# Kernel optimization log

Measured on AMD Instinct MI355X. Metric: run time of the kernel, lower is better.

Reference implementation:

```python
import jax, jax.numpy as jnp
import numpy as np

NUM_NODES = 100000
IN_DIM = 64
OUT_DIM = 64
NUM_EDGES = 1250000


def setup_inputs() -> dict:
    key = jax.random.key(0)
    k1, k2, k3, k4, k5 = jax.random.split(key, 5)
    x = jax.random.normal(k1, (NUM_NODES, IN_DIM), dtype=jnp.float32)
    edge_index = jax.random.randint(k2, (2, NUM_EDGES), 0, NUM_NODES, dtype=jnp.int32)
    # Linear params (PyTorch default init: uniform(-1/sqrt(in), 1/sqrt(in)))
    bound = 1.0 / np.sqrt(IN_DIM)
    W_self = jax.random.uniform(k3, (OUT_DIM, IN_DIM), minval=-bound, maxval=bound, dtype=jnp.float32)
    b_self = jax.random.uniform(k4, (OUT_DIM,), minval=-bound, maxval=bound, dtype=jnp.float32)
    W_neigh = jax.random.uniform(k5, (OUT_DIM, IN_DIM), minval=-bound, maxval=bound, dtype=jnp.float32)
    return {"x": x, "edge_index": edge_index, "W_self": W_self, "b_self": b_self, "W_neigh": W_neigh}


def reference(x, edge_index, W_self, b_self, W_neigh):
    # x: [N, D_in], edge_index: [2, E]
    src, dst = edge_index[0], edge_index[1]
    num_nodes = x.shape[0]
    x_src = x[src]  # [E, D_in] gather
    neigh_agg = jax.ops.segment_sum(x_src, dst, num_segments=num_nodes)  # [N, D_in]
    deg = jax.ops.segment_sum(jnp.ones_like(dst, dtype=x.dtype), dst, num_segments=num_nodes)
    deg = jnp.clip(deg, 1.0, None)[:, None]
    neigh_mean = neigh_agg / deg
    out = x @ W_self.T + b_self + neigh_mean @ W_neigh.T
    return jax.nn.relu(out)
```

## Files before the change

kernel.cpp:

```cpp
#include <hip/hip_runtime.h>


#define BKSH 9
#define BKN 512
#define NBMAX 256
#define CAPE 7168
#define WPT (CAPE / BKN)
#define CHUNK 4096
#define EPT (CHUNK / 256)

typedef __attribute__((ext_vector_type(8))) short short8;
typedef __attribute__((ext_vector_type(4))) float floatx4;

static __device__ inline unsigned short f2bf(float f) {
  union { float f; unsigned int u; } v;
  v.f = f;
  unsigned int r = v.u + 0x7FFFu + ((v.u >> 16) & 1u);
  return (unsigned short)(r >> 16);
}

static __device__ inline short8 pack8(float4 a, float4 b) {
  short8 s;
  s[0] = (short)f2bf(a.x); s[1] = (short)f2bf(a.y);
  s[2] = (short)f2bf(a.z); s[3] = (short)f2bf(a.w);
  s[4] = (short)f2bf(b.x); s[5] = (short)f2bf(b.y);
  s[6] = (short)f2bf(b.z); s[7] = (short)f2bf(b.w);
  return s;
}

static __device__ inline void add8(float* a, short8 sv) {
  union { short8 s; unsigned int u[4]; } c; c.s = sv;
#pragma unroll
  for (int i = 0; i < 4; ++i) {
    a[2 * i]     += __uint_as_float(c.u[i] << 16);
    a[2 * i + 1] += __uint_as_float(c.u[i] & 0xFFFF0000u);
  }
}

__global__ __launch_bounds__(256) void k1_main(
    const float* __restrict__ x,
    const float* __restrict__ Wself, const float* __restrict__ bself,
    const float* __restrict__ Wneigh,
    float* __restrict__ yb, unsigned short* __restrict__ zb,
    const int* __restrict__ src, const int* __restrict__ dst,
    int* __restrict__ cursor, int* __restrict__ ebuf,
    int E, int N, int NB, int SCB) {
  __shared__ int h[NBMAX], loff[NBMAX], gbase[NBMAX];
  __shared__ int sbuf[CHUNK];
  int t = threadIdx.x;
  int bid = blockIdx.x;

  if (bid >= SCB) {
    int lane = t & 63;
    int w = t >> 6;
    int tb = (bid - SCB) * 64 + w * 16;
    int m = lane & 15, q = lane >> 4;

    long long rowA = (long long)min(tb + m, N - 1) * 64;
    short8 ax[2];
#pragma unroll
    for (int ks = 0; ks < 2; ++ks) {
      const float* xr = &x[rowA + ks * 32 + q * 8];
      ax[ks] = pack8(*(const float4*)xr, *(const float4*)(xr + 4));
    }

#pragma unroll
    for (int nt = 0; nt < 4; ++nt) {
      int ob = nt * 16;
      long long rowB = (long long)(ob + m) * 64;
      floatx4 accs = {0.f, 0.f, 0.f, 0.f};
      floatx4 accn = {0.f, 0.f, 0.f, 0.f};
#pragma unroll
      for (int ks = 0; ks < 2; ++ks) {
        const float* pw = &Wself[rowB + ks * 32 + q * 8];
        short8 bs = pack8(*(const float4*)pw, *(const float4*)(pw + 4));
        accs = __builtin_amdgcn_mfma_f32_16x16x32_bf16(ax[ks], bs, accs, 0, 0, 0);
        const float* pn = &Wneigh[rowB + ks * 32 + q * 8];
        short8 bn = pack8(*(const float4*)pn, *(const float4*)(pn + 4));
        accn = __builtin_amdgcn_mfma_f32_16x16x32_bf16(ax[ks], bn, accn, 0, 0, 0);
      }
      float bias = bself[ob + m];
#pragma unroll
      for (int r = 0; r < 4; ++r) {
        int node = tb + q * 4 + r;
        if (node < N) {
          yb[(long long)node * 64 + ob + m] = accs[r] + bias;
          zb[(long long)node * 64 + ob + m] = f2bf(accn[r]);
        }
      }
    }
    return;
  }

  if (t < NBMAX) h[t] = 0;
  __syncthreads();

  int base = bid * CHUNK;
  int myd[EPT], mys[EPT];
#pragma unroll
  for (int i = 0; i < EPT; ++i) {
    int e = base + t + 256 * i;
    if (e < E) {
      myd[i] = dst[e];
      mys[i] = src[e];
      atomicAdd(&h[myd[i] >> BKSH], 1);
    } else myd[i] = -1;
  }
  __syncthreads();

  if (t < 64) {
    int i0 = 4 * t;
    int v0 = h[i0], v1 = h[i0 + 1], v2 = h[i0 + 2], v3 = h[i0 + 3];
    int s4 = v0 + v1 + v2 + v3, inc = s4;
#pragma unroll
    for (int off = 1; off < 64; off <<= 1) {
      int u = __shfl_up(inc, off, 64);
      if (t >= off) inc += u;
    }
    int ex = inc - s4;
    loff[i0] = ex; loff[i0 + 1] = ex + v0;
    loff[i0 + 2] = ex + v0 + v1; loff[i0 + 3] = ex + v0 + v1 + v2;
  }
  __syncthreads();

  if (t < NB) {
    if (h[t] > 0) gbase[t] = t * CAPE + atomicAdd(&cursor[t], h[t]);
  }
  if (t < NBMAX) h[t] = 0;
  __syncthreads();

#pragma unroll
  for (int i = 0; i < EPT; ++i) {
    if (myd[i] >= 0) {
      int b = myd[i] >> BKSH;
      int p = atomicAdd(&h[b], 1);
      sbuf[loff[b] + p] = mys[i] | ((myd[i] & (BKN - 1)) << 17);
    }
  }
  __syncthreads();

  int w = t >> 6, lane = t & 63;
  for (int b = w; b < NB; b += 4) {
    int c = h[b], lo = loff[b], go = gbase[b];
    for (int j = lane; j < c; j += 64)
      ebuf[go + j] = sbuf[lo + j];
  }
}

__global__ __launch_bounds__(512) void sb_csr(const int* __restrict__ cursor,
                                              const int* __restrict__ ebuf,
                                              int* __restrict__ col,
                                              int2* __restrict__ rowse, int N) {
  __shared__ int sbuf[CAPE];
  __shared__ int cnt[BKN];
  __shared__ int wsum[8];
  int b = blockIdx.x, t = threadIdx.x;
  int s = b * CAPE;
  int n = cursor[b];
  int e = s + n;

  int my[WPT];
#pragma unroll
  for (int i = 0; i < WPT; ++i) {
    int j = s + t + i * BKN;
    my[i] = (j < e) ? ebuf[j] : -1;
  }

  cnt[t] = 0;
  __syncthreads();
#pragma unroll
  for (int i = 0; i < WPT; ++i)
    if (my[i] >= 0) atomicAdd(&cnt[(my[i] >> 17) & (BKN - 1)], 1);
  __syncthreads();

  int v = cnt[t];
  int lane = t & 63, w = t >> 6;
  int inc = v;
#pragma unroll
  for (int o = 1; o < 64; o <<= 1) {
    int u = __shfl_up(inc, o, 64);
    if (lane >= o) inc += u;
  }
  if (lane == 63) wsum[w] = inc;
  __syncthreads();
  if (t < 8) {
    int s0 = wsum[t], incw = s0;
#pragma unroll
    for (int o = 1; o < 8; o <<= 1) {
      int u = __shfl_up(incw, o, 64);
      if (t >= o) incw += u;
    }
    wsum[t] = incw - s0;
  }
  __syncthreads();
  int ex = wsum[w] + inc - v;
  int node = (b << BKSH) + t;
  if (node < N) rowse[node] = make_int2(s + ex, v);
  __syncthreads();
  cnt[t] = ex;
  __syncthreads();

#pragma unroll
  for (int i = 0; i < WPT; ++i) {
    if (my[i] >= 0) {
      int nl = (my[i] >> 17) & (BKN - 1);
      int p = atomicAdd(&cnt[nl], 1);
      sbuf[p] = my[i] & 0x1FFFF;
    }
  }
  __syncthreads();

  for (int j = t; j < n; j += BKN) col[s + j] = sbuf[j];
}

__global__ __launch_bounds__(256) void gather_final(
    const unsigned short* __restrict__ zb,
    const int2* __restrict__ rowse,
    const int* __restrict__ col,
    const float* __restrict__ yb,
    float* __restrict__ out, int N) {
  int gid = blockIdx.x * 256 + threadIdx.x;
  int node = gid >> 6;
  if (node >= N) return;
  int lane = threadIdx.x & 63;
  int o = lane >> 3, d = lane & 7;
  int2 se = rowse[node];
  int s = se.x, c = se.y, e = s + c;

  float a[8] = {0.f, 0.f, 0.f, 0.f, 0.f, 0.f, 0.f, 0.f};
  float b2[8] = {0.f, 0.f, 0.f, 0.f, 0.f, 0.f, 0.f, 0.f};
  for (int j = s + o; j < e; j += 16) {
    int c0 = col[j];
    bool h2 = (j + 8) < e;
    int c1 = h2 ? col[j + 8] : c0;
    short8 v0 = *(const short8*)&zb[(long long)c0 * 64 + d * 8];
    short8 v1 = *(const short8*)&zb[(long long)c1 * 64 + d * 8];
    add8(a, v0);
    if (h2) add8(b2, v1);
  }
#pragma unroll
  for (int k = 0; k < 8; ++k) a[k] += b2[k];

#pragma unroll
  for (int m = 8; m <= 32; m <<= 1) {
#pragma unroll
    for (int k = 0; k < 8; ++k) a[k] += __shfl_xor(a[k], m, 64);
  }

  if (o == 0) {
    float inv = 1.0f / fmaxf((float)c, 1.0f);
    long long ro = (long long)node * 64 + d * 8;
    float4 y0 = *(const float4*)&yb[ro];
    float4 y1 = *(const float4*)&yb[ro + 4];
    float4 r0, r1;
    r0.x = fmaxf(y0.x + a[0] * inv, 0.f);
    r0.y = fmaxf(y0.y + a[1] * inv, 0.f);
    r0.z = fmaxf(y0.z + a[2] * inv, 0.f);
    r0.w = fmaxf(y0.w + a[3] * inv, 0.f);
    r1.x = fmaxf(y1.x + a[4] * inv, 0.f);
    r1.y = fmaxf(y1.y + a[5] * inv, 0.f);
    r1.z = fmaxf(y1.z + a[6] * inv, 0.f);
    r1.w = fmaxf(y1.w + a[7] * inv, 0.f);
    *(float4*)&out[ro] = r0;
    *(float4*)&out[ro + 4] = r1;
  }
}

extern "C" void kernel_launch(void* const* d_in, const int* in_sizes, int n_in,
                              void* d_out, int out_size, void* d_ws, size_t ws_size,
                              hipStream_t stream) {
  const float* x      = (const float*)d_in[0];
  const int*   eidx   = (const int*)d_in[1];
  const float* Wself  = (const float*)d_in[2];
  const float* bself  = (const float*)d_in[3];
  const float* Wneigh = (const float*)d_in[4];
  float* out = (float*)d_out;

  const int N = in_sizes[0] / 64;
  const int E = in_sizes[1] / 2;
  const int* src = eidx;
  const int* dst = eidx + E;
  const int NB = (N + BKN - 1) / BKN;

  float* yb = (float*)d_ws;
  unsigned short* zb = (unsigned short*)(yb + (size_t)N * 64);
  int* cursor = (int*)(zb + (size_t)N * 64);
  int2* rowse = (int2*)(cursor + NBMAX);
  int* ebuf   = (int*)(rowse + N);
  int* col    = ebuf + (size_t)NB * CAPE;

  hipMemsetAsync(cursor, 0, NBMAX * sizeof(int), stream);

  const int SCB = (E + CHUNK - 1) / CHUNK;
  const int GB = (N + 63) / 64;
  k1_main<<<SCB + GB, 256, 0, stream>>>(x, Wself, bself, Wneigh, yb, zb,
                                        src, dst, cursor, ebuf, E, N, NB, SCB);
  sb_csr<<<NB, BKN, 0, stream>>>(cursor, ebuf, col, rowse, N);
  gather_final<<<(int)(((long long)N * 64 + 255) / 256), 256, 0, stream>>>(
      zb, rowse, col, yb, out, N);
}
```

Before: 163.0 us.

## Replace two-pass bucketed CSR build with degree histogram, scan, and atomic scatter

Replaces the LDS-staged chunk bucketing and per-bucket local sort with a simpler CSR build. Per-node degrees are counted with global atomics, a per-bucket prefix scan produces row starts and cursors, and each edge is placed with a global atomicAdd on its destination cursor. This removes the intermediate ebuf pass and its shared-memory sorting. In exchange it uses 1.25M scattered global atomics, and neighbor order within a row becomes nondeterministic.

```diff
diff --git a/kernel.cpp b/kernel.cpp
--- a/kernel.cpp
+++ b/kernel.cpp
@@ -3,11 +3,8 @@
 
 #define BKSH 9
 #define BKN 512
-#define NBMAX 256
 #define CAPE 7168
-#define WPT (CAPE / BKN)
-#define CHUNK 4096
-#define EPT (CHUNK / 256)
+#define HISTB 512
 
 typedef __attribute__((ext_vector_type(8))) short short8;
 typedef __attribute__((ext_vector_type(4))) float floatx4;
@@ -42,138 +39,66 @@
     const float* __restrict__ Wself, const float* __restrict__ bself,
     const float* __restrict__ Wneigh,
     float* __restrict__ yb, unsigned short* __restrict__ zb,
-    const int* __restrict__ src, const int* __restrict__ dst,
-    int* __restrict__ cursor, int* __restrict__ ebuf,
-    int E, int N, int NB, int SCB) {
-  __shared__ int h[NBMAX], loff[NBMAX], gbase[NBMAX];
-  __shared__ int sbuf[CHUNK];
+    const int* __restrict__ dst, int* __restrict__ deg,
+    int E, int N) {
   int t = threadIdx.x;
   int bid = blockIdx.x;
 
-  if (bid >= SCB) {
-    int lane = t & 63;
-    int w = t >> 6;
-    int tb = (bid - SCB) * 64 + w * 16;
-    int m = lane & 15, q = lane >> 4;
-
-    long long rowA = (long long)min(tb + m, N - 1) * 64;
-    short8 ax[2];
+  if (bid < HISTB) {
+    int stride = HISTB * 256;
+    for (int e = bid * 256 + t; e < E; e += stride)
+      atomicAdd(&deg[dst[e]], 1);
+    return;
+  }
+
+  int lane = t & 63;
+  int w = t >> 6;
+  int tb = (bid - HISTB) * 64 + w * 16;
+  int m = lane & 15, q = lane >> 4;
+
+  long long rowA = (long long)min(tb + m, N - 1) * 64;
+  short8 ax[2];
+#pragma unroll
+  for (int ks = 0; ks < 2; ++ks) {
+    const float* xr = &x[rowA + ks * 32 + q * 8];
+    ax[ks] = pack8(*(const float4*)xr, *(const float4*)(xr + 4));
+  }
+
+#pragma unroll
+  for (int nt = 0; nt < 4; ++nt) {
+    int ob = nt * 16;
+    long long rowB = (long long)(ob + m) * 64;
+    floatx4 accs = {0.f, 0.f, 0.f, 0.f};
+    floatx4 accn = {0.f, 0.f, 0.f, 0.f};
 #pragma unroll
     for (int ks = 0; ks < 2; ++ks) {
-      const float* xr = &x[rowA + ks * 32 + q * 8];
-      ax[ks] = pack8(*(const float4*)xr, *(const float4*)(xr + 4));
+      const float* pw = &Wself[rowB + ks * 32 + q * 8];
+      short8 bs = pack8(*(const float4*)pw, *(const float4*)(pw + 4));
+      accs = __builtin_amdgcn_mfma_f32_16x16x32_bf16(ax[ks], bs, accs, 0, 0, 0);
+      const float* pn = &Wneigh[rowB + ks * 32 + q * 8];
+      short8 bn = pack8(*(const float4*)pn, *(const float4*)(pn + 4));
+      accn = __builtin_amdgcn_mfma_f32_16x16x32_bf16(ax[ks], bn, accn, 0, 0, 0);
     }
-
-#pragma unroll
-    for (int nt = 0; nt < 4; ++nt) {
-      int ob = nt * 16;
-      long long rowB = (long long)(ob + m) * 64;
-      floatx4 accs = {0.f, 0.f, 0.f, 0.f};
-      floatx4 accn = {0.f, 0.f, 0.f, 0.f};
-#pragma unroll
-      for (int ks = 0; ks < 2; ++ks) {
-        const float* pw = &Wself[rowB + ks * 32 + q * 8];
-        short8 bs = pack8(*(const float4*)pw, *(const float4*)(pw + 4));
-        accs = __builtin_amdgcn_mfma_f32_16x16x32_bf16(ax[ks], bs, accs, 0, 0, 0);
-        const float* pn = &Wneigh[rowB + ks * 32 + q * 8];
-        short8 bn = pack8(*(const float4*)pn, *(const float4*)(pn + 4));
-        accn = __builtin_amdgcn_mfma_f32_16x16x32_bf16(ax[ks], bn, accn, 0, 0, 0);
-      }
-      float bias = bself[ob + m];
-#pragma unroll
-      for (int r = 0; r < 4; ++r) {
-        int node = tb + q * 4 + r;
-        if (node < N) {
-          yb[(long long)node * 64 + ob + m] = accs[r] + bias;
-          zb[(long long)node * 64 + ob + m] = f2bf(accn[r]);
-        }
+    float bias = bself[ob + m];
+#pragma unroll
+    for (int r = 0; r < 4; ++r) {
+      int node = tb + q * 4 + r;
+      if (node < N) {
+        yb[(long long)node * 64 + ob + m] = accs[r] + bias;
+        zb[(long long)node * 64 + ob + m] = f2bf(accn[r]);
       }
     }
-    return;
-  }
-
-  if (t < NBMAX) h[t] = 0;
-  __syncthreads();
-
-  int base = bid * CHUNK;
-  int myd[EPT], mys[EPT];
-#pragma unroll
-  for (int i = 0; i < EPT; ++i) {
-    int e = base + t + 256 * i;
-    if (e < E) {
-      myd[i] = dst[e];
-      mys[i] = src[e];
-      atomicAdd(&h[myd[i] >> BKSH], 1);
-    } else myd[i] = -1;
-  }
-  __syncthreads();
-
-  if (t < 64) {
-    int i0 = 4 * t;
-    int v0 = h[i0], v1 = h[i0 + 1], v2 = h[i0 + 2], v3 = h[i0 + 3];
-    int s4 = v0 + v1 + v2 + v3, inc = s4;
-#pragma unroll
-    for (int off = 1; off < 64; off <<= 1) {
-      int u = __shfl_up(inc, off, 64);
-      if (t >= off) inc += u;
-    }
-    int ex = inc - s4;
-    loff[i0] = ex; loff[i0 + 1] = ex + v0;
-    loff[i0 + 2] = ex + v0 + v1; loff[i0 + 3] = ex + v0 + v1 + v2;
-  }
-  __syncthreads();
-
-  if (t < NB) {
-    if (h[t] > 0) gbase[t] = t * CAPE + atomicAdd(&cursor[t], h[t]);
-  }
-  if (t < NBMAX) h[t] = 0;
-  __syncthreads();
-
-#pragma unroll
-  for (int i = 0; i < EPT; ++i) {
-    if (myd[i] >= 0) {
-      int b = myd[i] >> BKSH;
-      int p = atomicAdd(&h[b], 1);
-      sbuf[loff[b] + p] = mys[i] | ((myd[i] & (BKN - 1)) << 17);
-    }
-  }
-  __syncthreads();
-
-  int w = t >> 6, lane = t & 63;
-  for (int b = w; b < NB; b += 4) {
-    int c = h[b], lo = loff[b], go = gbase[b];
-    for (int j = lane; j < c; j += 64)
-      ebuf[go + j] = sbuf[lo + j];
-  }
-}
-
-__global__ __launch_bounds__(512) void sb_csr(const int* __restrict__ cursor,
-                                              const int* __restrict__ ebuf,
-                                              int* __restrict__ col,
-                                              int2* __restrict__ rowse, int N) {
-  __shared__ int sbuf[CAPE];
-  __shared__ int cnt[BKN];
+  }
+}
+
+__global__ __launch_bounds__(512) void bucket_scan(const int* __restrict__ deg,
+                                                   int2* __restrict__ rowse,
+                                                   int* __restrict__ cur, int N) {
   __shared__ int wsum[8];
   int b = blockIdx.x, t = threadIdx.x;
-  int s = b * CAPE;
-  int n = cursor[b];
-  int e = s + n;
-
-  int my[WPT];
-#pragma unroll
-  for (int i = 0; i < WPT; ++i) {
-    int j = s + t + i * BKN;
-    my[i] = (j < e) ? ebuf[j] : -1;
-  }
-
-  cnt[t] = 0;
-  __syncthreads();
-#pragma unroll
-  for (int i = 0; i < WPT; ++i)
-    if (my[i] >= 0) atomicAdd(&cnt[(my[i] >> 17) & (BKN - 1)], 1);
-  __syncthreads();
-
-  int v = cnt[t];
+  int node = (b << BKSH) + t;
+  int v = (node < N) ? deg[node] : 0;
+
   int lane = t & 63, w = t >> 6;
   int inc = v;
 #pragma unroll
@@ -194,23 +119,22 @@
   }
   __syncthreads();
   int ex = wsum[w] + inc - v;
-  int node = (b << BKSH) + t;
-  if (node < N) rowse[node] = make_int2(s + ex, v);
-  __syncthreads();
-  cnt[t] = ex;
-  __syncthreads();
-
-#pragma unroll
-  for (int i = 0; i < WPT; ++i) {
-    if (my[i] >= 0) {
-      int nl = (my[i] >> 17) & (BKN - 1);
-      int p = atomicAdd(&cnt[nl], 1);
-      sbuf[p] = my[i] & 0x1FFFF;
-    }
-  }
-  __syncthreads();
-
-  for (int j = t; j < n; j += BKN) col[s + j] = sbuf[j];
+  int start = b * CAPE + ex;
+  if (node < N) {
+    rowse[node] = make_int2(start, v);
+    cur[node] = start;
+  }
+}
+
+__global__ __launch_bounds__(256) void edge_scatter(const int* __restrict__ src,
+                                                    const int* __restrict__ dst,
+                                                    int* __restrict__ cur,
+                                                    int* __restrict__ col, int E) {
+  int e = blockIdx.x * 256 + threadIdx.x;
+  if (e < E) {
+    int p = atomicAdd(&cur[dst[e]], 1);
+    col[p] = src[e];
+  }
 }
 
 __global__ __launch_bounds__(256) void gather_final(
@@ -284,18 +208,18 @@
 
   float* yb = (float*)d_ws;
   unsigned short* zb = (unsigned short*)(yb + (size_t)N * 64);
-  int* cursor = (int*)(zb + (size_t)N * 64);
-  int2* rowse = (int2*)(cursor + NBMAX);
-  int* ebuf   = (int*)(rowse + N);
-  int* col    = ebuf + (size_t)NB * CAPE;
-
-  hipMemsetAsync(cursor, 0, NBMAX * sizeof(int), stream);
-
-  const int SCB = (E + CHUNK - 1) / CHUNK;
+  int* deg    = (int*)(zb + (size_t)N * 64);
+  int* cur    = deg + N;
+  int2* rowse = (int2*)(cur + N);
+  int* col    = (int*)(rowse + N);
+
+  hipMemsetAsync(deg, 0, (size_t)N * sizeof(int), stream);
+
   const int GB = (N + 63) / 64;
-  k1_main<<<SCB + GB, 256, 0, stream>>>(x, Wself, bself, Wneigh, yb, zb,
-                                        src, dst, cursor, ebuf, E, N, NB, SCB);
-  sb_csr<<<NB, BKN, 0, stream>>>(cursor, ebuf, col, rowse, N);
+  k1_main<<<HISTB + GB, 256, 0, stream>>>(x, Wself, bself, Wneigh, yb, zb,
+                                          dst, deg, E, N);
+  bucket_scan<<<NB, BKN, 0, stream>>>(deg, rowse, cur, N);
+  edge_scatter<<<(E + 255) / 256, 256, 0, stream>>>(src, dst, cur, col, E);
   gather_final<<<(int)(((long long)N * 64 + 255) / 256), 256, 0, stream>>>(
       zb, rowse, col, yb, out, N);
 }
```

After: 288.6 us. 1.77x slower.
